# Optimization experiments

Measured on AMD Instinct MI355X. Metric: run time of the kernel, lower is better.

The kernel has to match this reference:

```python
import jax, jax.numpy as jnp
import numpy as np

def setup_inputs() -> dict:
    key = jax.random.key(0)
    k1, k2, k3 = jax.random.split(key, 3)
    B, L, H, E = 2, 2048, 16, 64
    queries = jax.random.normal(k1, (B, L, H, E), dtype=jnp.float32)
    keys = jax.random.normal(k2, (B, L, H, E), dtype=jnp.float32)
    values = jax.random.normal(k3, (B, L, H, E), dtype=jnp.float32)
    return {"queries": queries, "keys": keys, "values": values}

def reference(queries, keys, values):
    B, L, H, E = queries.shape
    S = keys.shape[1]
    scale = 1.0 / jnp.sqrt(jnp.asarray(E, dtype=queries.dtype))
    # scores: [B, H, L, S]
    scores = jnp.einsum('blhe,bshe->bhls', queries, keys)
    # causal mask: position l attends to s <= l (TriangularCausalMask triu diag=1 is masked)
    causal = jnp.tril(jnp.ones((L, S), dtype=bool))  # True = keep
    scores = jnp.where(causal[None, None, :, :], scores, -jnp.inf)
    A = jax.nn.softmax(scale * scores, axis=-1)
    # dropout is identity in eval / p=0
    V = jnp.einsum('bhls,bshd->blhd', A, values)
    return V
```

## Files before the change

### kernel.cpp

```cpp
#include <hip/hip_runtime.h>
#include <hip/hip_bf16.h>

typedef __attribute__((ext_vector_type(8))) short short8;
typedef __attribute__((ext_vector_type(4))) float f32x4;
typedef __attribute__((ext_vector_type(2))) unsigned uint2v;

#define MFMA16(a, b, c) __builtin_amdgcn_mfma_f32_16x16x32_bf16((a), (b), (c), 0, 0, 0)

constexpr int Bc = 2, Lc = 2048, Hc = 16, Ec = 64;
constexpr float LOG2E = 1.4426950408889634f;
constexpr float SCALE2 = 0.125f * LOG2E;
constexpr float NEGBIG = -3.0e38f;

union SW { short8 s8; unsigned u[4]; float4 f4; };

__device__ __forceinline__ unsigned cvtpk(float lo, float hi) {
  unsigned r;
  asm("v_cvt_pk_bf16_f32 %0, %1, %2" : "=v"(r) : "v"(lo), "v"(hi));
  return r;
}
__device__ __forceinline__ float exp2v(float x) {
  float r;
  asm("v_exp_f32 %0, %1" : "=v"(r) : "v"(x));
  return r;
}
__device__ __forceinline__ void plswap32(unsigned& a, unsigned& b) {
  uint2v r = __builtin_amdgcn_permlane32_swap(a, b, false, false);
  a = r[0]; b = r[1];
}
__device__ __forceinline__ void plswap16(unsigned& a, unsigned& b) {
  uint2v r = __builtin_amdgcn_permlane16_swap(a, b, false, false);
  a = r[0]; b = r[1];
}
__device__ __forceinline__ float bflymax(float x) {
  unsigned a = __builtin_bit_cast(unsigned, x), b = a;
  plswap16(a, b);
  float y = fmaxf(__builtin_bit_cast(float, a), __builtin_bit_cast(float, b));
  a = __builtin_bit_cast(unsigned, y); b = a;
  plswap32(a, b);
  return fmaxf(__builtin_bit_cast(float, a), __builtin_bit_cast(float, b));
}

__global__ __launch_bounds__(256)
void prep(const float* __restrict__ K, const float* __restrict__ V,
          uint4* __restrict__ Kb, unsigned short* __restrict__ Vt) {
  const int bid = blockIdx.x;
  const int t = threadIdx.x;
  if (bid < 2048) {
    const int i = bid * 256 + t;
    const float4* s = reinterpret_cast<const float4*>(K) + (size_t)i * 2;
    float4 a = s[0], b = s[1];
    uint4 o;
    o.x = cvtpk(a.x, a.y); o.y = cvtpk(a.z, a.w);
    o.z = cvtpk(b.x, b.y); o.w = cvtpk(b.z, b.w);
    Kb[i] = o;
  } else {
    const int vw = (bid - 2048) * 4 + (t >> 6);
    const int l = t & 63;
    const int bh = vw >> 7;
    const int s0 = (vw & 127) * 16;
    const float* vp = V + ((size_t)(bh >> 4) * Lc + s0) * (Hc * Ec) +
                      (bh & 15) * Ec + l;
    float va[16];
    #pragma unroll
    for (int j = 0; j < 16; ++j) va[j] = vp[j * (Hc * Ec)];
    uint4 o0, o1;
    o0.x = cvtpk(va[0], va[1]);   o0.y = cvtpk(va[2], va[3]);
    o0.z = cvtpk(va[4], va[5]);   o0.w = cvtpk(va[6], va[7]);
    o1.x = cvtpk(va[8], va[9]);   o1.y = cvtpk(va[10], va[11]);
    o1.z = cvtpk(va[12], va[13]); o1.w = cvtpk(va[14], va[15]);
    uint4* dst = reinterpret_cast<uint4*>(Vt + ((size_t)vw * 64 + l) * 16);
    dst[0] = o0;
    dst[1] = o1;
  }
}

__global__ __launch_bounds__(512, 2)
void attn_fwd(const float* __restrict__ Qg, const unsigned short* __restrict__ Kb,
              const unsigned short* __restrict__ Vt, float* __restrict__ Og) {
  __shared__ __align__(16) short smem[32768];

  const int bid = blockIdx.x;
  const int pair = bid >> 5;
  const int bh = bid & 31;
  const int h = bh & (Hc - 1);
  const int b = bh >> 4;
  const int iLo = pair;
  const int QbL = iLo * 64;
  const int QbH = (31 - pair) * 64;
  const int RL = (iLo + 2) >> 1;

  const int t = threadIdx.x;
  const int w = t >> 6;
  const int qsub = w & 3;
  const int par = w >> 2;
  const int l = t & 63;
  const int n = l & 15;
  const int g = l >> 4;
  const int sp4 = ((g & 1) << 3) | ((g >> 1) << 2);

  const f32x4 zero4 = {0.f, 0.f, 0.f, 0.f};
  short8 onesv;
  #pragma unroll
  for (int j = 0; j < 8; ++j) onesv[j] = (short)0x3F80;

  short8 qf[2];
  auto loadq = [&](int Qb) {
    const int q = Qb + qsub * 16 + n;
    const float* qp = Qg + ((size_t)(b * Lc + q) * Hc + h) * Ec + g * 8;
    SW a0, a1, b0, b1, r0, r1;
    a0.f4 = reinterpret_cast<const float4*>(qp)[0];
    a1.f4 = reinterpret_cast<const float4*>(qp)[1];
    b0.f4 = reinterpret_cast<const float4*>(qp + 32)[0];
    b1.f4 = reinterpret_cast<const float4*>(qp + 32)[1];
    r0.u[0] = cvtpk(a0.f4.x * SCALE2, a0.f4.y * SCALE2);
    r0.u[1] = cvtpk(a0.f4.z * SCALE2, a0.f4.w * SCALE2);
    r0.u[2] = cvtpk(a1.f4.x * SCALE2, a1.f4.y * SCALE2);
    r0.u[3] = cvtpk(a1.f4.z * SCALE2, a1.f4.w * SCALE2);
    r1.u[0] = cvtpk(b0.f4.x * SCALE2, b0.f4.y * SCALE2);
    r1.u[1] = cvtpk(b0.f4.z * SCALE2, b0.f4.w * SCALE2);
    r1.u[2] = cvtpk(b1.f4.x * SCALE2, b1.f4.y * SCALE2);
    r1.u[3] = cvtpk(b1.f4.z * SCALE2, b1.f4.w * SCALE2);
    qf[0] = r0.s8;
    qf[1] = r1.s8;
  };

  f32x4 acc[4] = {zero4, zero4, zero4, zero4};
  float mrun = NEGBIG, lrun = 0.f;

  const int srow = t >> 2;
  const int prow = (srow & ~12) | ((srow & 4) << 1) | ((srow & 8) >> 1);
  const int kc0 = (t & 3) * 16;
  const int ve = l, vs0 = w * 16;

  float4 kA, kB, vA, vB;

  auto issue = [&](int r0) {
    unsigned koff = (unsigned)((((b * Lc + r0 + srow) * Hc + h) * Ec + kc0) * 2);
    unsigned voff = (unsigned)(((bh * 128 + ((r0 + vs0) >> 4)) * 64 + ve) * 32);
    asm volatile(
      "global_load_dwordx4 %[k0], %[ko], %[kb]\n\t"
      "global_load_dwordx4 %[k1], %[ko], %[kb] offset:16\n\t"
      "global_load_dwordx4 %[v0], %[vo], %[vb]\n\t"
      "global_load_dwordx4 %[v1], %[vo], %[vb] offset:16"
      : [k0]"=v"(kA), [k1]"=v"(kB), [v0]"=v"(vA), [v1]"=v"(vB)
      : [ko]"v"(koff), [vo]"v"(voff), [kb]"s"(Kb), [vb]"s"(Vt)
      : "memory");
  };
  auto commit = [&](int buf) {
    asm volatile("s_waitcnt vmcnt(2)" ::: "memory");
    __builtin_amdgcn_sched_barrier(0);
    short* kt = smem + buf * 8192;
    *reinterpret_cast<short8*>(&kt[(prow * 64 + kc0) ^ ((prow & 7) << 3)]) =
        *reinterpret_cast<short8*>(&kA);
    *reinterpret_cast<short8*>(&kt[(prow * 64 + kc0 + 8) ^ ((prow & 7) << 3)]) =
        *reinterpret_cast<short8*>(&kB);
    asm volatile("s_waitcnt vmcnt(0)" ::: "memory");
    __builtin_amdgcn_sched_barrier(0);
    short* vt = smem + 16384 + buf * 8192;
    const int ch0 = vs0 >> 3;
    *reinterpret_cast<short8*>(&vt[ve * 128 + (((ch0 + 0) ^ (ve & 7)) << 3)]) =
        *reinterpret_cast<short8*>(&vA);
    *reinterpret_cast<short8*>(&vt[ve * 128 + (((ch0 + 1) ^ (ve & 7)) << 3)]) =
        *reinterpret_cast<short8*>(&vB);
  };

  auto round = [&](int Qb, int str, int curb) {
    const int sb = str * 128 + par * 64;
    const int qtop = Qb + qsub * 16;
    if (sb > qtop + 15) return;
    const short* ktb = smem + curb * 8192;
    const short* vtb = smem + 16384 + curb * 8192;

    f32x4 sc[4] = {zero4, zero4, zero4, zero4};
    __builtin_amdgcn_s_setprio(1);
    #pragma unroll
    for (int kc = 0; kc < 2; ++kc) {
      #pragma unroll
      for (int cb = 0; cb < 4; ++cb) {
        const int row = par * 64 + cb * 16 + n;
        const int idx = (row * 64 + kc * 32 + g * 8) ^ ((n & 7) << 3);
        short8 kf = *reinterpret_cast<const short8*>(&ktb[idx]);
        sc[cb] = MFMA16(kf, qf[kc], sc[cb]);
      }
    }
    __builtin_amdgcn_s_setprio(0);

    const int qg = qtop + n;
    if (sb + 63 > qtop) {
      #pragma unroll
      for (int cb = 0; cb < 4; ++cb)
        #pragma unroll
        for (int r = 0; r < 4; ++r)
          if (sb + cb * 16 + sp4 + r > qg) sc[cb][r] = NEGBIG;
    }

    float m8 = fmaxf(fmaxf(fmaxf(sc[0][0], sc[0][1]), fmaxf(sc[0][2], sc[0][3])),
                     fmaxf(fmaxf(sc[1][0], sc[1][1]), fmaxf(sc[1][2], sc[1][3])));
    m8 = fmaxf(m8, fmaxf(fmaxf(fmaxf(sc[2][0], sc[2][1]), fmaxf(sc[2][2], sc[2][3])),
                         fmaxf(fmaxf(sc[3][0], sc[3][1]), fmaxf(sc[3][2], sc[3][3]))));
    m8 = bflymax(m8);

    const bool resc = !__all(m8 <= mrun);
    if (resc) {
      const float mn = fmaxf(mrun, m8);
      const float afac = exp2v(mrun - mn);
      mrun = mn;
      lrun *= afac;
      #pragma unroll
      for (int e4 = 0; e4 < 4; ++e4)
        #pragma unroll
        for (int r = 0; r < 4; ++r) acc[e4][r] *= afac;
    }

    unsigned ua[4], ub[4];
    #pragma unroll
    for (int cb = 0; cb < 4; ++cb) {
      ua[cb] = cvtpk(exp2v(sc[cb][0] - mrun), exp2v(sc[cb][1] - mrun));
      ub[cb] = cvtpk(exp2v(sc[cb][2] - mrun), exp2v(sc[cb][3] - mrun));
    }

    plswap32(ua[0], ua[1]);
    plswap32(ub[0], ub[1]);
    plswap32(ua[2], ua[3]);
    plswap32(ub[2], ub[3]);
    SW pw0, pw1;
    pw0.u[0] = ua[0]; pw0.u[1] = ub[0]; pw0.u[2] = ua[1]; pw0.u[3] = ub[1];
    pw1.u[0] = ua[2]; pw1.u[1] = ub[2]; pw1.u[2] = ua[3]; pw1.u[3] = ub[3];

    __builtin_amdgcn_s_setprio(1);
    #pragma unroll
    for (int e4 = 0; e4 < 4; ++e4) {
      const int e = e4 * 16 + n;
      const int slot0 = (par * 8 + g) ^ (e & 7);
      const int slot1 = (par * 8 + 4 + g) ^ (e & 7);
      short8 vf0 = *reinterpret_cast<const short8*>(&vtb[e * 128 + (slot0 << 3)]);
      acc[e4] = MFMA16(vf0, pw0.s8, acc[e4]);
      short8 vf1 = *reinterpret_cast<const short8*>(&vtb[e * 128 + (slot1 << 3)]);
      acc[e4] = MFMA16(vf1, pw1.s8, acc[e4]);
    }
    f32x4 rs = MFMA16(onesv, pw0.s8, zero4);
    rs = MFMA16(onesv, pw1.s8, rs);
    __builtin_amdgcn_s_setprio(0);
    lrun += rs[0];
  };

  auto merge_store = [&](int Qb, int curb) {
    float* sA = reinterpret_cast<float*>(smem) + curb * 4096;
    float* sB = reinterpret_cast<float*>(smem) + 8192 + curb * 4096;
    __syncthreads();
    const int row = qsub * 16 + n;
    if (par == 1) {
      float* base = (row < 32) ? (sA + row * 68) : (sB + (row - 32) * 68);
      #pragma unroll
      for (int e4 = 0; e4 < 4; ++e4)
        #pragma unroll
        for (int r = 0; r < 4; ++r) base[e4 * 16 + g * 4 + r] = acc[e4][r];
      if (g == 0) {
        sB[2176 + row] = mrun;
        sB[2240 + row] = lrun;
      }
    }
    __syncthreads();
    if (par == 0) {
      const float* base = (row < 32) ? (sA + row * 68) : (sB + (row - 32) * 68);
      const float m1 = sB[2176 + row];
      const float l1 = sB[2240 + row];
      const float mm = fmaxf(mrun, m1);
      const float a0 = exp2v(mrun - mm);
      const float a1 = exp2v(m1 - mm);
      const float inv = 1.0f / (lrun * a0 + l1 * a1);
      const int q = Qb + row;
      float* op = Og + ((size_t)(b * Lc + q) * Hc + h) * Ec;
      #pragma unroll
      for (int e4 = 0; e4 < 4; ++e4) {
        float4 v;
        v.x = (acc[e4][0] * a0 + base[e4 * 16 + g * 4 + 0] * a1) * inv;
        v.y = (acc[e4][1] * a0 + base[e4 * 16 + g * 4 + 1] * a1) * inv;
        v.z = (acc[e4][2] * a0 + base[e4 * 16 + g * 4 + 2] * a1) * inv;
        v.w = (acc[e4][3] * a0 + base[e4 * 16 + g * 4 + 3] * a1) * inv;
        *reinterpret_cast<float4*>(op + e4 * 16 + g * 4) = v;
      }
    }
  };

  constexpr int NRO = 17;
  loadq(QbL);
  issue(0);
  commit(0);
  __syncthreads();

  int cur = 0;
  for (int rd = 0; rd < NRO; ++rd) {
    const bool pre = (rd + 1 < NRO);
    if (pre) {
      const int nrd = rd + 1;
      const int nstr = (nrd < RL) ? nrd : nrd - RL;
      issue(nstr * 128);
    }
    const bool lo = (rd < RL);
    round(lo ? QbL : QbH, lo ? rd : rd - RL, cur);
    if (rd == RL - 1) {
      merge_store(QbL, cur);
      #pragma unroll
      for (int e4 = 0; e4 < 4; ++e4) acc[e4] = zero4;
      mrun = NEGBIG;
      lrun = 0.f;
      loadq(QbH);
    }
    if (pre) commit(cur ^ 1);
    __syncthreads();
    cur ^= 1;
  }

  merge_store(QbH, cur ^ 1);
}

extern "C" void kernel_launch(void* const* d_in, const int* in_sizes, int n_in,
                              void* d_out, int out_size, void* d_ws, size_t ws_size,
                              hipStream_t stream) {
  const float* Q = (const float*)d_in[0];
  const float* K = (const float*)d_in[1];
  const float* V = (const float*)d_in[2];
  float* O = (float*)d_out;
  unsigned short* Kb = (unsigned short*)d_ws;
  unsigned short* Vt = (unsigned short*)((char*)d_ws + (size_t)Bc * Lc * Hc * Ec * 2);
  prep<<<dim3(3072), dim3(256), 0, stream>>>(K, V, (uint4*)Kb, Vt);
  dim3 grid(Bc * Hc * 16);
  attn_fwd<<<grid, dim3(512), 0, stream>>>(Q, Kb, Vt, O);
}
```

Baseline: 49.11 us.

## Load V fragments directly from global into registers instead of staging through LDS

V tiles are no longer copied into shared memory. Each wave now issues per-round global loads of its V MFMA operand fragments straight into registers, overlapping them with the QK^T MFMAs and softmax, and only K is still double-buffered in LDS. The next K tile is prefetched after the V loads, and the waitcnt is placed so that only the V loads have to complete before the PV MFMAs. This roughly halves LDS use and removes the V LDS writes and reads, at the cost of more global/L2 traffic, since each wave fetches V separately, and more VGPRs for the fragments.

```diff
diff --git a/kernel.cpp b/kernel.cpp
--- a/kernel.cpp
+++ b/kernel.cpp
@@ -78,7 +78,8 @@
 __global__ __launch_bounds__(512, 2)
 void attn_fwd(const float* __restrict__ Qg, const unsigned short* __restrict__ Kb,
               const unsigned short* __restrict__ Vt, float* __restrict__ Og) {
-  __shared__ __align__(16) short smem[32768];
+  __shared__ __align__(16) short kt2[2][8192];
+  __shared__ __align__(16) float mscr[64 * 68 + 128];
 
   const int bid = blockIdx.x;
   const int pair = bid >> 5;
@@ -131,46 +132,36 @@
   const int srow = t >> 2;
   const int prow = (srow & ~12) | ((srow & 4) << 1) | ((srow & 8) >> 1);
   const int kc0 = (t & 3) * 16;
-  const int ve = l, vs0 = w * 16;
-
-  float4 kA, kB, vA, vB;
-
-  auto issue = [&](int r0) {
+
+  float4 kA, kB;
+
+  auto issueK = [&](int r0) {
     unsigned koff = (unsigned)((((b * Lc + r0 + srow) * Hc + h) * Ec + kc0) * 2);
-    unsigned voff = (unsigned)(((bh * 128 + ((r0 + vs0) >> 4)) * 64 + ve) * 32);
     asm volatile(
       "global_load_dwordx4 %[k0], %[ko], %[kb]\n\t"
-      "global_load_dwordx4 %[k1], %[ko], %[kb] offset:16\n\t"
-      "global_load_dwordx4 %[v0], %[vo], %[vb]\n\t"
-      "global_load_dwordx4 %[v1], %[vo], %[vb] offset:16"
-      : [k0]"=v"(kA), [k1]"=v"(kB), [v0]"=v"(vA), [v1]"=v"(vB)
-      : [ko]"v"(koff), [vo]"v"(voff), [kb]"s"(Kb), [vb]"s"(Vt)
+      "global_load_dwordx4 %[k1], %[ko], %[kb] offset:16"
+      : [k0]"=v"(kA), [k1]"=v"(kB)
+      : [ko]"v"(koff), [kb]"s"(Kb)
       : "memory");
   };
   auto commit = [&](int buf) {
-    asm volatile("s_waitcnt vmcnt(2)" ::: "memory");
+    asm volatile("s_waitcnt vmcnt(0)" ::: "memory");
     __builtin_amdgcn_sched_barrier(0);
-    short* kt = smem + buf * 8192;
+    short* kt = kt2[buf];
     *reinterpret_cast<short8*>(&kt[(prow * 64 + kc0) ^ ((prow & 7) << 3)]) =
         *reinterpret_cast<short8*>(&kA);
     *reinterpret_cast<short8*>(&kt[(prow * 64 + kc0 + 8) ^ ((prow & 7) << 3)]) =
         *reinterpret_cast<short8*>(&kB);
-    asm volatile("s_waitcnt vmcnt(0)" ::: "memory");
-    __builtin_amdgcn_sched_barrier(0);
-    short* vt = smem + 16384 + buf * 8192;
-    const int ch0 = vs0 >> 3;
-    *reinterpret_cast<short8*>(&vt[ve * 128 + (((ch0 + 0) ^ (ve & 7)) << 3)]) =
-        *reinterpret_cast<short8*>(&vA);
-    *reinterpret_cast<short8*>(&vt[ve * 128 + (((ch0 + 1) ^ (ve & 7)) << 3)]) =
-        *reinterpret_cast<short8*>(&vB);
-  };
-
-  auto round = [&](int Qb, int str, int curb) {
+  };
+
+  auto round = [&](int Qb, int str, int curb, bool pre, int nstrK) {
     const int sb = str * 128 + par * 64;
     const int qtop = Qb + qsub * 16;
-    if (sb > qtop + 15) return;
-    const short* ktb = smem + curb * 8192;
-    const short* vtb = smem + 16384 + curb * 8192;
+    if (sb > qtop + 15) {
+      if (pre) issueK(nstrK * 128);
+      return;
+    }
+    const short* ktb = kt2[curb];
 
     f32x4 sc[4] = {zero4, zero4, zero4, zero4};
     __builtin_amdgcn_s_setprio(1);
@@ -186,6 +177,27 @@
     }
     __builtin_amdgcn_s_setprio(0);
 
+    SW vr0[4], vr1[4];
+    {
+      unsigned a0 = (unsigned)((((bh * 128 + str * 8 + par * 4 + (g >> 1)) * 64 + n) * 32)
+                               + ((g & 1) * 16));
+      unsigned a1 = a0 + 4096;
+      asm volatile(
+        "global_load_dwordx4 %[f0], %[a0], %[vb]\n\t"
+        "global_load_dwordx4 %[f1], %[a0], %[vb] offset:512\n\t"
+        "global_load_dwordx4 %[f2], %[a0], %[vb] offset:1024\n\t"
+        "global_load_dwordx4 %[f3], %[a0], %[vb] offset:1536\n\t"
+        "global_load_dwordx4 %[f4], %[a1], %[vb]\n\t"
+        "global_load_dwordx4 %[f5], %[a1], %[vb] offset:512\n\t"
+        "global_load_dwordx4 %[f6], %[a1], %[vb] offset:1024\n\t"
+        "global_load_dwordx4 %[f7], %[a1], %[vb] offset:1536"
+        : [f0]"=v"(vr0[0].f4), [f1]"=v"(vr0[1].f4), [f2]"=v"(vr0[2].f4), [f3]"=v"(vr0[3].f4),
+          [f4]"=v"(vr1[0].f4), [f5]"=v"(vr1[1].f4), [f6]"=v"(vr1[2].f4), [f7]"=v"(vr1[3].f4)
+        : [a0]"v"(a0), [a1]"v"(a1), [vb]"s"(Vt)
+        : "memory");
+    }
+    if (pre) issueK(nstrK * 128);
+
     const int qg = qtop + n;
     if (sb + 63 > qtop) {
       #pragma unroll
@@ -219,7 +231,6 @@
       ua[cb] = cvtpk(exp2v(sc[cb][0] - mrun), exp2v(sc[cb][1] - mrun));
       ub[cb] = cvtpk(exp2v(sc[cb][2] - mrun), exp2v(sc[cb][3] - mrun));
     }
-
     plswap32(ua[0], ua[1]);
     plswap32(ub[0], ub[1]);
     plswap32(ua[2], ua[3]);
@@ -228,16 +239,15 @@
     pw0.u[0] = ua[0]; pw0.u[1] = ub[0]; pw0.u[2] = ua[1]; pw0.u[3] = ub[1];
     pw1.u[0] = ua[2]; pw1.u[1] = ub[2]; pw1.u[2] = ua[3]; pw1.u[3] = ub[3];
 
+    if (pre) asm volatile("s_waitcnt vmcnt(2)" ::: "memory");
+    else     asm volatile("s_waitcnt vmcnt(0)" ::: "memory");
+    __builtin_amdgcn_sched_barrier(0);
+
     __builtin_amdgcn_s_setprio(1);
     #pragma unroll
     for (int e4 = 0; e4 < 4; ++e4) {
-      const int e = e4 * 16 + n;
-      const int slot0 = (par * 8 + g) ^ (e & 7);
-      const int slot1 = (par * 8 + 4 + g) ^ (e & 7);
-      short8 vf0 = *reinterpret_cast<const short8*>(&vtb[e * 128 + (slot0 << 3)]);
-      acc[e4] = MFMA16(vf0, pw0.s8, acc[e4]);
-      short8 vf1 = *reinterpret_cast<const short8*>(&vtb[e * 128 + (slot1 << 3)]);
-      acc[e4] = MFMA16(vf1, pw1.s8, acc[e4]);
+      acc[e4] = MFMA16(vr0[e4].s8, pw0.s8, acc[e4]);
+      acc[e4] = MFMA16(vr1[e4].s8, pw1.s8, acc[e4]);
     }
     f32x4 rs = MFMA16(onesv, pw0.s8, zero4);
     rs = MFMA16(onesv, pw1.s8, rs);
@@ -245,27 +255,25 @@
     lrun += rs[0];
   };
 
-  auto merge_store = [&](int Qb, int curb) {
-    float* sA = reinterpret_cast<float*>(smem) + curb * 4096;
-    float* sB = reinterpret_cast<float*>(smem) + 8192 + curb * 4096;
+  auto merge_store = [&](int Qb) {
     __syncthreads();
     const int row = qsub * 16 + n;
     if (par == 1) {
-      float* base = (row < 32) ? (sA + row * 68) : (sB + (row - 32) * 68);
+      float* base = mscr + row * 68;
       #pragma unroll
       for (int e4 = 0; e4 < 4; ++e4)
         #pragma unroll
         for (int r = 0; r < 4; ++r) base[e4 * 16 + g * 4 + r] = acc[e4][r];
       if (g == 0) {
-        sB[2176 + row] = mrun;
-        sB[2240 + row] = lrun;
+        mscr[64 * 68 + row] = mrun;
+        mscr[64 * 68 + 64 + row] = lrun;
       }
     }
     __syncthreads();
     if (par == 0) {
-      const float* base = (row < 32) ? (sA + row * 68) : (sB + (row - 32) * 68);
-      const float m1 = sB[2176 + row];
-      const float l1 = sB[2240 + row];
+      const float* base = mscr + row * 68;
+      const float m1 = mscr[64 * 68 + row];
+      const float l1 = mscr[64 * 68 + 64 + row];
       const float mm = fmaxf(mrun, m1);
       const float a0 = exp2v(mrun - mm);
       const float a1 = exp2v(m1 - mm);
@@ -286,22 +294,19 @@
 
   constexpr int NRO = 17;
   loadq(QbL);
-  issue(0);
+  issueK(0);
   commit(0);
   __syncthreads();
 
   int cur = 0;
   for (int rd = 0; rd < NRO; ++rd) {
     const bool pre = (rd + 1 < NRO);
-    if (pre) {
-      const int nrd = rd + 1;
-      const int nstr = (nrd < RL) ? nrd : nrd - RL;
-      issue(nstr * 128);
-    }
+    const int nrd = rd + 1;
+    const int nstr = (nrd < RL) ? nrd : nrd - RL;
     const bool lo = (rd < RL);
-    round(lo ? QbL : QbH, lo ? rd : rd - RL, cur);
+    round(lo ? QbL : QbH, lo ? rd : rd - RL, cur, pre, nstr);
     if (rd == RL - 1) {
-      merge_store(QbL, cur);
+      merge_store(QbL);
       #pragma unroll
       for (int e4 = 0; e4 < 4; ++e4) acc[e4] = zero4;
       mrun = NEGBIG;
@@ -313,7 +318,7 @@
     cur ^= 1;
   }
 
-  merge_store(QbH, cur ^ 1);
+  merge_store(QbH);
 }
 
 extern "C" void kernel_launch(void* const* d_in, const int* in_sizes, int n_in,
```

Measured after the change: 50.38 us. 2.6% more time.
